# Optimization experiments

Measured on AMD Instinct MI355X. Metric: run time of the kernel, lower is better.

The kernel has to match this reference:

```python
import jax, jax.numpy as jnp
import numpy as np

T, B = 128, 64
EMB, HID, NTOK = 400, 1152, 33278
# layer dims: (in, out) per layer, matching AWD_LSTM construction
LAYER_DIMS = [(EMB, HID), (HID, HID), (HID, EMB)]


def _uniform(key, shape, bound):
    return jax.random.uniform(key, shape, jnp.float32, -bound, bound)


def setup_inputs() -> dict:
    key = jax.random.key(0)
    ks = jax.random.split(key, 32)
    inp = {
        "x": jax.random.normal(ks[0], (T, B, EMB), jnp.float32),
        "h0_0": jnp.zeros((B, HID), jnp.float32),
        "h0_1": jnp.zeros((B, HID), jnp.float32),
        "h0_2": jnp.zeros((B, EMB), jnp.float32),
        "c0_0": jnp.zeros((B, HID), jnp.float32),
        "c0_1": jnp.zeros((B, HID), jnp.float32),
        "c0_2": jnp.zeros((B, EMB), jnp.float32),
    }
    ki = 1
    for li, (din, dout) in enumerate(LAYER_DIMS):
        bound = 1.0 / np.sqrt(dout)
        inp[f"W_ih{li}"] = _uniform(ks[ki + 0], (4 * dout, din), bound)
        inp[f"W_hh{li}"] = _uniform(ks[ki + 1], (4 * dout, dout), bound)
        inp[f"b_ih{li}"] = _uniform(ks[ki + 2], (4 * dout,), bound)
        inp[f"b_hh{li}"] = _uniform(ks[ki + 3], (4 * dout,), bound)
        ki += 4
    bd = 1.0 / np.sqrt(EMB)
    inp["W_dec"] = _uniform(ks[ki], (NTOK, EMB), bd)
    inp["b_dec"] = _uniform(ks[ki + 1], (NTOK,), bd)
    return inp


def _lstm_cell(x, h, c, W_ih, W_hh, b_ih, b_hh):
    # PyTorch gate order: i, f, g, o
    gates = x @ W_ih.T + b_ih + h @ W_hh.T + b_hh
    i, f, g, o = jnp.split(gates, 4, axis=-1)
    c_new = jax.nn.sigmoid(f) * c + jax.nn.sigmoid(i) * jnp.tanh(g)
    h_new = jax.nn.sigmoid(o) * jnp.tanh(c_new)
    return h_new, c_new


def reference(x, h0_0, h0_1, h0_2, c0_0, c0_1, c0_2,
              W_ih0, W_hh0, b_ih0, b_hh0,
              W_ih1, W_hh1, b_ih1, b_hh1,
              W_ih2, W_hh2, b_ih2, b_hh2,
              W_dec, b_dec):
    params = [(W_ih0, W_hh0, b_ih0, b_hh0),
              (W_ih1, W_hh1, b_ih1, b_hh1),
              (W_ih2, W_hh2, b_ih2, b_hh2)]

    def step(carry, xt):
        hs, cs = carry
        inp = xt
        new_h, new_c = [], []
        for li in range(3):
            h, c = _lstm_cell(inp, hs[li], cs[li], *params[li])
            new_h.append(h)
            new_c.append(c)
            inp = h
        return (tuple(new_h), tuple(new_c)), new_h[-1]

    carry0 = ((h0_0, h0_1, h0_2), (c0_0, c0_1, c0_2))
    (hs, cs), out = jax.lax.scan(step, carry0, x)  # out: (T, B, EMB)
    decoded = out.reshape(T * B, EMB) @ W_dec.T + b_dec
    return decoded.reshape(T, B, NTOK)
```

## Files before the change

kernel.cpp:

```cpp
#include <hip/hip_runtime.h>
#include <math.h>

typedef unsigned short u16;
typedef __attribute__((ext_vector_type(8))) short short8;
typedef __attribute__((ext_vector_type(4))) float f32x4;
typedef __attribute__((ext_vector_type(2))) float f32x2;

__device__ __forceinline__ u16 f32_to_bf16(float x) {
    union { float f; unsigned int u; } v; v.f = x;
    unsigned int u = v.u;
    return (u16)((u + 0x7FFFu + ((u >> 16) & 1u)) >> 16);
}
__device__ __forceinline__ float bf16_to_f32(u16 h) {
    union { unsigned int u; float f; } v; v.u = ((unsigned int)h) << 16; return v.f;
}

__global__ void split_pad_kernel(const float* __restrict__ src,
                                 u16* __restrict__ hi, u16* __restrict__ lo,
                                 int N, int K, int Npad, int Kpad, int perm)
{
    int idx = blockIdx.x * 256 + threadIdx.x;
    if (idx >= Npad * Kpad) return;
    int n = idx / Kpad, k = idx - n * Kpad;
    float x = 0.f;
    if (n < N && k < K) {
        int srow = n;
        if (perm) { int dout = N >> 2; srow = (n & 3) * dout + (n >> 2); }
        x = src[(size_t)srow * K + k];
    }
    u16 h = f32_to_bf16(x);
    hi[idx] = h;
    lo[idx] = f32_to_bf16(x - bf16_to_f32(h));
}

__global__ void bias_perm_kernel(const float* __restrict__ bi,
                                 const float* __restrict__ bh,
                                 float* __restrict__ out, int N4)
{
    int c = blockIdx.x * 256 + threadIdx.x;
    if (c >= N4) return;
    int dout = N4 >> 2;
    int s = (c & 3) * dout + (c >> 2);
    out[c] = bi[s] + bh[s];
}

__global__ __launch_bounds__(256) void gemm3m(
    const float* __restrict__ Af32,
    const u16* __restrict__ Ahi, const u16* __restrict__ Alo,
    const u16* __restrict__ Whi, const u16* __restrict__ Wlo,
    const float* __restrict__ bias,
    float* __restrict__ C,
    int Nreal, int Kreal, int Kp, int lda, int ldc, int amode,
    int MT, int NSUB)
{
    extern __shared__ __align__(16) char smem[];
    u16 (*As)[128][32] = (u16 (*)[128][32])smem;
    u16 (*Ws)[128][32] = (u16 (*)[128][32])(smem + 16384);
    float (*Cs)[129]   = (float (*)[129])smem;

    const int tid  = threadIdx.x;
    const int lane = tid & 63, wave = tid >> 6;

    const int bid   = blockIdx.x;
    const int super = bid / (NSUB * MT);
    const int rem   = bid - super * (NSUB * MT);
    const int mtile = rem / NSUB;
    const int ntile = super * NSUB + (rem - mtile * NSUB);
    const int m0 = mtile * 128, n0 = ntile * 128;

    const int wm = (wave >> 1) * 64, wn = (wave & 1) * 64;

    f32x4 acc[4][4];
#pragma unroll
    for (int i = 0; i < 4; ++i)
#pragma unroll
        for (int j = 0; j < 4; ++j)
#pragma unroll
            for (int r = 0; r < 4; ++r) acc[i][j][r] = 0.f;

    const int srow = tid >> 2;
    const int sq   = tid & 3;
    const int dq   = (sq ^ ((srow >> 2) & 3)) * 8;
    const int fr   = lane & 15;
    const int fq   = lane >> 4;
    const int rcol = (fq ^ ((fr >> 2) & 3)) * 8;

    for (int k0 = 0; k0 < Kp; k0 += 32) {
#pragma unroll
        for (int half = 0; half < 2; ++half) {
            int row = half * 64 + srow;
            int kc  = k0 + sq * 8;
            if (amode == 0) {
                union { u16 s[8]; short8 v; } uh, ul;
                if (kc + 8 <= Kreal) {
                    const float* p = &Af32[(size_t)(m0 + row) * lda + kc];
#pragma unroll
                    for (int j = 0; j < 8; ++j) {
                        float xv = p[j];
                        u16 hh = f32_to_bf16(xv);
                        uh.s[j] = hh;
                        ul.s[j] = f32_to_bf16(xv - bf16_to_f32(hh));
                    }
                } else {
#pragma unroll
                    for (int j = 0; j < 8; ++j) { uh.s[j] = 0; ul.s[j] = 0; }
                }
                *(short8*)&As[0][row][dq] = uh.v;
                *(short8*)&As[1][row][dq] = ul.v;
            } else {
                size_t ao = (size_t)(m0 + row) * lda + kc;
                *(short8*)&As[0][row][dq] = *(const short8*)(Ahi + ao);
                *(short8*)&As[1][row][dq] = *(const short8*)(Alo + ao);
            }
            size_t wo = (size_t)(n0 + row) * Kp + kc;
            *(short8*)&Ws[0][row][dq] = *(const short8*)(Whi + wo);
            *(short8*)&Ws[1][row][dq] = *(const short8*)(Wlo + wo);
        }
        __syncthreads();

        short8 ah[4], al[4], wh[4], wl[4];
#pragma unroll
        for (int f = 0; f < 4; ++f) {
            int arow = wm + f * 16 + fr;
            ah[f] = *(const short8*)&As[0][arow][rcol];
            al[f] = *(const short8*)&As[1][arow][rcol];
            int wrow = wn + f * 16 + fr;
            wh[f] = *(const short8*)&Ws[0][wrow][rcol];
            wl[f] = *(const short8*)&Ws[1][wrow][rcol];
        }
#pragma unroll
        for (int i = 0; i < 4; ++i)
#pragma unroll
            for (int j = 0; j < 4; ++j) {
                acc[i][j] = __builtin_amdgcn_mfma_f32_16x16x32_bf16(ah[i], wh[j], acc[i][j], 0, 0, 0);
                acc[i][j] = __builtin_amdgcn_mfma_f32_16x16x32_bf16(ah[i], wl[j], acc[i][j], 0, 0, 0);
                acc[i][j] = __builtin_amdgcn_mfma_f32_16x16x32_bf16(al[i], wh[j], acc[i][j], 0, 0, 0);
            }
        __syncthreads();
    }

    const int erow = tid & 31;
    const int echk = tid >> 5;
    const int gm_base = m0 + ((erow >> 4) * 64) + (erow & 15);
    const int gn0 = n0 + echk * 16;
    const bool vec4ok = ((ldc & 3) == 0);

#pragma unroll
    for (int i = 0; i < 4; ++i) {
        __syncthreads();
#pragma unroll
        for (int j = 0; j < 4; ++j)
#pragma unroll
            for (int r = 0; r < 4; ++r)
                Cs[(wave >> 1) * 16 + fq * 4 + r][wn + j * 16 + fr] = acc[i][j][r];
        __syncthreads();

        const int gm = gm_base + i * 16;
        float* crow = C + (size_t)gm * ldc;
        if (gn0 + 16 <= Nreal) {
#pragma unroll
            for (int q = 0; q < 4; ++q) {
                f32x4 v = *(const f32x4*)&Cs[erow][echk * 16 + q * 4];
                if (bias) {
                    f32x4 bv = *(const f32x4*)&bias[gn0 + q * 4];
                    v += bv;
                }
                if (vec4ok) {
                    *(f32x4*)&crow[gn0 + q * 4] = v;
                } else {
                    f32x2 lo2 = {v[0], v[1]}, hi2 = {v[2], v[3]};
                    *(f32x2*)&crow[gn0 + q * 4]     = lo2;
                    *(f32x2*)&crow[gn0 + q * 4 + 2] = hi2;
                }
            }
        } else {
#pragma unroll
            for (int q = 0; q < 4; ++q)
#pragma unroll
                for (int p = 0; p < 4; ++p) {
                    int n = gn0 + q * 4 + p;
                    if (n < Nreal)
                        crow[n] = Cs[erow][echk * 16 + q * 4 + p] + (bias ? bias[n] : 0.f);
                }
        }
    }
}

#define PF(S, KT_) do {                                                        \
    int q_ = (((KT_) * 4 + fq) ^ sxor) * 8;                                    \
    a0h_##S = *(const short8*)&Wlds[rA * Kp + q_];                             \
    a0l_##S = *(const short8*)&Wlds[(32 + rA) * Kp + q_];                      \
    a1h_##S = *(const short8*)&Wlds[rB * Kp + q_];                             \
    a1l_##S = *(const short8*)&Wlds[(32 + rB) * Kp + q_];                      \
    hh_##S = *(const short8*)(hrow_hi + (KT_) * 32 + fq * 8);                  \
    hl_##S = *(const short8*)(hrow_lo + (KT_) * 32 + fq * 8);                  \
} while (0)

#define CM(S) do {                                                             \
    accA = __builtin_amdgcn_mfma_f32_16x16x32_bf16(a0h_##S, hh_##S, accA, 0, 0, 0); \
    accB = __builtin_amdgcn_mfma_f32_16x16x32_bf16(a1h_##S, hh_##S, accB, 0, 0, 0); \
    accA = __builtin_amdgcn_mfma_f32_16x16x32_bf16(a0h_##S, hl_##S, accA, 0, 0, 0); \
    accB = __builtin_amdgcn_mfma_f32_16x16x32_bf16(a1h_##S, hl_##S, accB, 0, 0, 0); \
    accA = __builtin_amdgcn_mfma_f32_16x16x32_bf16(a0l_##S, hh_##S, accA, 0, 0, 0); \
    accB = __builtin_amdgcn_mfma_f32_16x16x32_bf16(a1l_##S, hh_##S, accB, 0, 0, 0); \
} while (0)

__global__ __launch_bounds__(256, 1) void persistent_lstm(
    const u16* __restrict__ Whi, const u16* __restrict__ Wlo,
    const u16* __restrict__ h0hi, const u16* __restrict__ h0lo,
    u16* __restrict__ seqHi, u16* __restrict__ seqLo,
    const float* __restrict__ pre,
    const float* __restrict__ c_in, float* __restrict__ c_out,
    int* __restrict__ gcnt,
    int t0, int N4, int Kp, int dout, int G)
{
    extern __shared__ __align__(16) u16 Wlds[];
    const int tid  = threadIdx.x;
    const int lane = tid & 63, wave = tid >> 6;
    const int fr = lane & 15, fq = lane >> 4;
    const int c0blk = blockIdx.x * 32;
    const int CH = Kp >> 3;
    const int b = wave * 16 + fr;
    const int grp = blockIdx.x & 7;

    for (int idx = tid; idx < 64 * CH; idx += 256) {
        int buf = idx / (32 * CH);
        int rem = idx - buf * 32 * CH;
        int r = rem / CH, q = rem - r * CH;
        const u16* src = buf ? Wlo : Whi;
        short8 v = *(const short8*)(src + (size_t)(c0blk + r) * Kp + q * 8);
        *(short8*)&Wlds[(buf * 32 + r) * Kp + (q ^ (r & 7)) * 8] = v;
    }

    const int cA = c0blk + fq * 4;
    const int cB = cA + 16;
    const int jA = cA >> 2, jB = cB >> 2;
    float cregA = c_in[(size_t)b * dout + jA];
    float cregB = c_in[(size_t)b * dout + jB];

    const int rA = fr, rB = 16 + fr;
    const int sxor = fr & 7;
    const int KT = Kp >> 5;

    f32x4 preA = *(const f32x4*)(pre + (size_t)b * N4 + cA);
    f32x4 preB = *(const f32x4*)(pre + (size_t)b * N4 + cB);
    __syncthreads();

    for (int ts = 0; ts < 64; ++ts) {
        const int t = t0 + ts;
        const u16* hbase_hi = (t == 0) ? h0hi : seqHi + (size_t)(t - 1) * 64 * Kp;
        const u16* hbase_lo = (t == 0) ? h0lo : seqLo + (size_t)(t - 1) * 64 * Kp;
        const u16* hrow_hi = hbase_hi + (size_t)b * Kp;
        const u16* hrow_lo = hbase_lo + (size_t)b * Kp;

        f32x4 accA = {0.f, 0.f, 0.f, 0.f};
        f32x4 accB = {0.f, 0.f, 0.f, 0.f};
        short8 a0h_0, a0l_0, a1h_0, a1l_0, hh_0, hl_0;
        short8 a0h_1, a0l_1, a1h_1, a1l_1, hh_1, hl_1;
        short8 a0h_2, a0l_2, a1h_2, a1l_2, hh_2, hl_2;
        short8 a0h_3, a0l_3, a1h_3, a1l_3, hh_3, hl_3;
        short8 a0h_4, a0l_4, a1h_4, a1l_4, hh_4, hl_4;
        short8 a0h_5, a0l_5, a1h_5, a1l_5, hh_5, hl_5;

        PF(0, 0); PF(1, 1); PF(2, 2); PF(3, 3); PF(4, 4); PF(5, 5);
        for (int kt = 0; kt < KT - 6; kt += 6) {
            CM(0); PF(0, kt + 6);
            CM(1); PF(1, kt + 7);
            CM(2); PF(2, kt + 8);
            CM(3); PF(3, kt + 9);
            CM(4); PF(4, kt + 10);
            CM(5); PF(5, kt + 11);
        }
        CM(0); CM(1); CM(2); CM(3); CM(4); CM(5);

#pragma unroll
        for (int ct = 0; ct < 2; ++ct) {
            f32x4 a = ct ? accB : accA;
            f32x4 p = ct ? preB : preA;
            int j  = ct ? jB : jA;
            float gi = a[0] + p[0];
            float gf = a[1] + p[1];
            float gg = a[2] + p[2];
            float go_ = a[3] + p[3];
            float si = 1.f / (1.f + expf(-gi));
            float sf = 1.f / (1.f + expf(-gf));
            float so = 1.f / (1.f + expf(-go_));
            float tg = tanhf(gg);
            float cn = sf * (ct ? cregB : cregA) + si * tg;
            float hv = so * tanhf(cn);
            if (ct) cregB = cn; else cregA = cn;
            u16 hb = f32_to_bf16(hv);
            size_t so_ = (size_t)(t * 64 + b) * Kp + j;
            seqHi[so_] = hb;
            seqLo[so_] = f32_to_bf16(hv - bf16_to_f32(hb));
        }

        if (ts != 63) {
            __syncthreads();
            {
                const float* prow2 = pre + (size_t)((ts + 1) * 64 + b) * N4;
                preA = *(const f32x4*)(prow2 + cA);
                preB = *(const f32x4*)(prow2 + cB);
            }
            if (tid == 0) {
                __builtin_amdgcn_fence(__ATOMIC_RELEASE, "agent");
                __hip_atomic_fetch_add(&gcnt[(ts * 8 + grp) * 32], 1,
                                       __ATOMIC_RELAXED, __HIP_MEMORY_SCOPE_AGENT);
                int sum;
                do {
                    sum = 0;
#pragma unroll
                    for (int g = 0; g < 8; ++g)
                        sum += __hip_atomic_load(&gcnt[(ts * 8 + g) * 32],
                                                 __ATOMIC_RELAXED, __HIP_MEMORY_SCOPE_AGENT);
                    if (sum < G) __builtin_amdgcn_s_sleep(1);
                } while (sum < G);
            }
            __syncthreads();
            __builtin_amdgcn_sched_barrier(0);
        }
    }

    c_out[(size_t)b * dout + jA] = cregA;
    c_out[(size_t)b * dout + jB] = cregB;
}

extern "C" void kernel_launch(void* const* d_in, const int* in_sizes, int n_in,
                              void* d_out, int out_size, void* d_ws, size_t ws_size,
                              hipStream_t stream)
{
    const int T = 128, B = 64, EMB = 400, HID = 1152, NTOK = 33278;
    const int TB = T * B;

    const float* x     = (const float*)d_in[0];
    const float* h0[3] = {(const float*)d_in[1], (const float*)d_in[2], (const float*)d_in[3]};
    const float* c0[3] = {(const float*)d_in[4], (const float*)d_in[5], (const float*)d_in[6]};
    const float* W_ih[3] = {(const float*)d_in[7],  (const float*)d_in[11], (const float*)d_in[15]};
    const float* W_hh[3] = {(const float*)d_in[8],  (const float*)d_in[12], (const float*)d_in[16]};
    const float* b_ih[3] = {(const float*)d_in[9],  (const float*)d_in[13], (const float*)d_in[17]};
    const float* b_hh[3] = {(const float*)d_in[10], (const float*)d_in[14], (const float*)d_in[18]};
    const float* W_dec = (const float*)d_in[19];
    const float* b_dec = (const float*)d_in[20];

    const int din[3]    = {EMB, HID, HID};
    const int Kpre[3]   = {416, 1152, 1152};
    const int dh[3]     = {HID, HID, EMB};
    const int KpH[3]    = {1152, 1152, 576};
    const int N4[3]     = {4608, 4608, 1600};
    const int N4p128[3] = {4608, 4608, 1664};
    const int NSUBpre[3] = {6, 6, 13};
    const int Gp[3]     = {144, 144, 50};

    char* wsp = (char*)d_ws;
    size_t off = 0;
    auto alloc = [&](size_t bytes) -> char* {
        char* p = wsp + off; off = (off + bytes + 255) & ~(size_t)255; return p;
    };

    float* pre   = (float*)alloc((size_t)4096 * 4608 * 4);
    u16* seqHi   = (u16*)alloc((size_t)TB * 1152 * 2);
    u16* seqLo   = (u16*)alloc((size_t)TB * 1152 * 2);
    u16* WihHi   = (u16*)alloc((size_t)4608 * 1152 * 2);
    u16* WihLo   = (u16*)alloc((size_t)4608 * 1152 * 2);
    u16* WhhHi   = (u16*)alloc((size_t)4608 * 1152 * 2);
    u16* WhhLo   = (u16*)alloc((size_t)4608 * 1152 * 2);
    u16* h0Hi    = (u16*)alloc((size_t)B * 1152 * 2);
    u16* h0Lo    = (u16*)alloc((size_t)B * 1152 * 2);
    float* bsum  = (float*)alloc(4608 * 4);
    float* cstb  = (float*)alloc((size_t)B * HID * 4);
    const size_t gcntN = (size_t)6 * 64 * 8 * 32;
    int* gcnt = (int*)alloc(gcntN * 4);
    u16* WdecHi  = (u16*)pre;
    u16* WdecLo  = (u16*)pre + (size_t)33280 * 416;

    hipMemsetAsync(gcnt, 0, gcntN * 4, stream);
    hipFuncSetAttribute(reinterpret_cast<const void*>(persistent_lstm),
                        hipFuncAttributeMaxDynamicSharedMemorySize, 160 * 1024);
    hipFuncSetAttribute(reinterpret_cast<const void*>(gemm3m),
                        hipFuncAttributeMaxDynamicSharedMemorySize, 64 * 1024);

    auto run_split = [&](const float* src, u16* hi, u16* lo,
                         int N, int K, int Npad, int Kpad, int perm) {
        int total = Npad * Kpad;
        split_pad_kernel<<<(total + 255) / 256, 256, 0, stream>>>(
            src, hi, lo, N, K, Npad, Kpad, perm);
    };

    for (int l = 0; l < 3; ++l) {
        run_split(W_hh[l], WhhHi, WhhLo, N4[l], dh[l], N4[l], KpH[l], 1);
        run_split(h0[l], h0Hi, h0Lo, B, dh[l], B, KpH[l], 0);
        run_split(W_ih[l], WihHi, WihLo, N4[l], din[l], N4p128[l], Kpre[l], 1);
        bias_perm_kernel<<<(N4[l] + 255) / 256, 256, 0, stream>>>(
            b_ih[l], b_hh[l], bsum, N4[l]);

        const int ldaA = (l == 0) ? EMB : KpH[l - 1];
        const int NT = N4p128[l] / 128, MT = 32;
        const size_t ldsB = (size_t)128 * KpH[l];

        for (int halfT = 0; halfT < 2; ++halfT) {
            const int li = l * 2 + halfT;
            const float* Af32 = (l == 0) ? (x + (size_t)halfT * 4096 * EMB) : nullptr;
            const u16* Ah = (l == 0) ? nullptr : (seqHi + (size_t)halfT * 4096 * ldaA);
            const u16* Al = (l == 0) ? nullptr : (seqLo + (size_t)halfT * 4096 * ldaA);
            gemm3m<<<dim3(NT * MT), 256, 32768, stream>>>(
                Af32, Ah, Al, WihHi, WihLo, bsum, pre,
                N4[l], din[l], Kpre[l], ldaA, N4[l], (l == 0) ? 0 : 1,
                MT, NSUBpre[l]);

            const float* cin = (halfT == 0) ? c0[l] : cstb;
            persistent_lstm<<<dim3(Gp[l]), 256, ldsB, stream>>>(
                WhhHi, WhhLo, h0Hi, h0Lo, seqHi, seqLo, pre,
                cin, cstb,
                gcnt + (size_t)li * 64 * 8 * 32,
                halfT * 64, N4[l], KpH[l], dh[l], Gp[l]);
        }
    }

    run_split(W_dec, WdecHi, WdecLo, NTOK, EMB, 33280, 416, 0);
    gemm3m<<<dim3(260 * 64), 256, 32768, stream>>>(
        nullptr, seqHi, seqLo, WdecHi, WdecLo, b_dec, (float*)d_out,
        NTOK, EMB, 416, 576, NTOK, 1,
        64, 5);
}
```

Before: 6.536 ms.

## Use per-block flags, packed hi/lo hidden state, and LDS-direct loads in GEMM

Several changes land together. The LSTM grid barrier's grouped counters are replaced by one flag per block, each polled by its own thread. The hidden state is now stored as packed hi/lo u32 words written with atomic stores, so one load fetches both halves, and perm instructions split them apart. The GEMM's bf16 operand path now loads tiles directly into LDS through global_load_lds, one wave per buffer. The decoder GEMM's sub-tiling parameter also changes, and each step writes an extra sequence buffer, which adds memory traffic.

```diff
diff --git a/kernel.cpp b/kernel.cpp
--- a/kernel.cpp
+++ b/kernel.cpp
@@ -2,9 +2,11 @@
 #include <math.h>
 
 typedef unsigned short u16;
+typedef unsigned int u32;
 typedef __attribute__((ext_vector_type(8))) short short8;
 typedef __attribute__((ext_vector_type(4))) float f32x4;
 typedef __attribute__((ext_vector_type(2))) float f32x2;
+typedef __attribute__((ext_vector_type(4))) unsigned int u32x4;
 
 __device__ __forceinline__ u16 f32_to_bf16(float x) {
     union { float f; unsigned int u; } v; v.f = x;
@@ -13,6 +15,12 @@
 }
 __device__ __forceinline__ float bf16_to_f32(u16 h) {
     union { unsigned int u; float f; } v; v.u = ((unsigned int)h) << 16; return v.f;
+}
+
+__device__ __forceinline__ void gload16(const u16* g, u16* l) {
+    __builtin_amdgcn_global_load_lds(
+        (const __attribute__((address_space(1))) void*)g,
+        (__attribute__((address_space(3))) void*)l, 16, 0, 0);
 }
 
 __global__ void split_pad_kernel(const float* __restrict__ src,
@@ -33,6 +41,18 @@
     lo[idx] = f32_to_bf16(x - bf16_to_f32(h));
 }
 
+__global__ void pack_h0_kernel(const float* __restrict__ src, u32* __restrict__ dst,
+                               int Brows, int K, int Kpad)
+{
+    int idx = blockIdx.x * 256 + threadIdx.x;
+    if (idx >= Brows * Kpad) return;
+    int b = idx / Kpad, k = idx - b * Kpad;
+    float x = (k < K) ? src[(size_t)b * K + k] : 0.f;
+    u16 h = f32_to_bf16(x);
+    u16 l = f32_to_bf16(x - bf16_to_f32(h));
+    dst[idx] = (u32)h | ((u32)l << 16);
+}
+
 __global__ void bias_perm_kernel(const float* __restrict__ bi,
                                  const float* __restrict__ bh,
                                  float* __restrict__ out, int N4)
@@ -85,12 +105,23 @@
     const int fq   = lane >> 4;
     const int rcol = (fq ^ ((fr >> 2) & 3)) * 8;
 
+    const u16* gb = nullptr; u16* lb = nullptr; int gstr = 0;
+    if (amode != 0) {
+        u16* AsB = (u16*)smem;
+        u16* WsB = (u16*)(smem + 16384);
+        if (wave == 0)      { gb = Ahi + (size_t)m0 * lda; gstr = lda; lb = AsB; }
+        else if (wave == 1) { gb = Alo + (size_t)m0 * lda; gstr = lda; lb = AsB + 4096; }
+        else if (wave == 2) { gb = Whi + (size_t)n0 * Kp;  gstr = Kp;  lb = WsB; }
+        else                { gb = Wlo + (size_t)n0 * Kp;  gstr = Kp;  lb = WsB + 4096; }
+    }
+    const int lrow = lane >> 2, lq = lane & 3;
+
     for (int k0 = 0; k0 < Kp; k0 += 32) {
-#pragma unroll
-        for (int half = 0; half < 2; ++half) {
-            int row = half * 64 + srow;
-            int kc  = k0 + sq * 8;
-            if (amode == 0) {
+        if (amode == 0) {
+#pragma unroll
+            for (int half = 0; half < 2; ++half) {
+                int row = half * 64 + srow;
+                int kc  = k0 + sq * 8;
                 union { u16 s[8]; short8 v; } uh, ul;
                 if (kc + 8 <= Kreal) {
                     const float* p = &Af32[(size_t)(m0 + row) * lda + kc];
@@ -107,14 +138,17 @@
                 }
                 *(short8*)&As[0][row][dq] = uh.v;
                 *(short8*)&As[1][row][dq] = ul.v;
-            } else {
-                size_t ao = (size_t)(m0 + row) * lda + kc;
-                *(short8*)&As[0][row][dq] = *(const short8*)(Ahi + ao);
-                *(short8*)&As[1][row][dq] = *(const short8*)(Alo + ao);
-            }
-            size_t wo = (size_t)(n0 + row) * Kp + kc;
-            *(short8*)&Ws[0][row][dq] = *(const short8*)(Whi + wo);
-            *(short8*)&Ws[1][row][dq] = *(const short8*)(Wlo + wo);
+                size_t wo = (size_t)(n0 + row) * Kp + k0 + sq * 8;
+                *(short8*)&Ws[0][row][dq] = *(const short8*)(Whi + wo);
+                *(short8*)&Ws[1][row][dq] = *(const short8*)(Wlo + wo);
+            }
+        } else {
+#pragma unroll
+            for (int g = 0; g < 8; ++g) {
+                int row = g * 16 + lrow;
+                int srcq = lq ^ ((row >> 2) & 3);
+                gload16(gb + (size_t)row * gstr + k0 + srcq * 8, lb + g * 512);
+            }
         }
         __syncthreads();
 
@@ -192,8 +226,18 @@
     a0l_##S = *(const short8*)&Wlds[(32 + rA) * Kp + q_];                      \
     a1h_##S = *(const short8*)&Wlds[rB * Kp + q_];                             \
     a1l_##S = *(const short8*)&Wlds[(32 + rB) * Kp + q_];                      \
-    hh_##S = *(const short8*)(hrow_hi + (KT_) * 32 + fq * 8);                  \
-    hl_##S = *(const short8*)(hrow_lo + (KT_) * 32 + fq * 8);                  \
+    u32x4 u0_ = *(const u32x4*)(hrow + (KT_) * 32 + fq * 8);                   \
+    u32x4 u1_ = *(const u32x4*)(hrow + (KT_) * 32 + fq * 8 + 4);               \
+    union { short8 v; u32 d[4]; } H_, L_;                                      \
+    H_.d[0] = __builtin_amdgcn_perm(u0_[1], u0_[0], 0x05040100u);              \
+    L_.d[0] = __builtin_amdgcn_perm(u0_[1], u0_[0], 0x07060302u);              \
+    H_.d[1] = __builtin_amdgcn_perm(u0_[3], u0_[2], 0x05040100u);              \
+    L_.d[1] = __builtin_amdgcn_perm(u0_[3], u0_[2], 0x07060302u);              \
+    H_.d[2] = __builtin_amdgcn_perm(u1_[1], u1_[0], 0x05040100u);              \
+    L_.d[2] = __builtin_amdgcn_perm(u1_[1], u1_[0], 0x07060302u);              \
+    H_.d[3] = __builtin_amdgcn_perm(u1_[3], u1_[2], 0x05040100u);              \
+    L_.d[3] = __builtin_amdgcn_perm(u1_[3], u1_[2], 0x07060302u);              \
+    hh_##S = H_.v; hl_##S = L_.v;                                              \
 } while (0)
 
 #define CM(S) do {                                                             \
@@ -207,11 +251,12 @@
 
 __global__ __launch_bounds__(256, 1) void persistent_lstm(
     const u16* __restrict__ Whi, const u16* __restrict__ Wlo,
-    const u16* __restrict__ h0hi, const u16* __restrict__ h0lo,
+    const u32* __restrict__ h0HL,
+    u32* __restrict__ seqHL,
     u16* __restrict__ seqHi, u16* __restrict__ seqLo,
     const float* __restrict__ pre,
     const float* __restrict__ c_in, float* __restrict__ c_out,
-    int* __restrict__ gcnt,
+    int* __restrict__ flags,
     int t0, int N4, int Kp, int dout, int G)
 {
     extern __shared__ __align__(16) u16 Wlds[];
@@ -221,7 +266,6 @@
     const int c0blk = blockIdx.x * 32;
     const int CH = Kp >> 3;
     const int b = wave * 16 + fr;
-    const int grp = blockIdx.x & 7;
 
     for (int idx = tid; idx < 64 * CH; idx += 256) {
         int buf = idx / (32 * CH);
@@ -248,10 +292,8 @@
 
     for (int ts = 0; ts < 64; ++ts) {
         const int t = t0 + ts;
-        const u16* hbase_hi = (t == 0) ? h0hi : seqHi + (size_t)(t - 1) * 64 * Kp;
-        const u16* hbase_lo = (t == 0) ? h0lo : seqLo + (size_t)(t - 1) * 64 * Kp;
-        const u16* hrow_hi = hbase_hi + (size_t)b * Kp;
-        const u16* hrow_lo = hbase_lo + (size_t)b * Kp;
+        const u32* hbase = (t == 0) ? h0HL : seqHL + (size_t)(t - 1) * 64 * Kp;
+        const u32* hrow = hbase + (size_t)b * Kp;
 
         f32x4 accA = {0.f, 0.f, 0.f, 0.f};
         f32x4 accB = {0.f, 0.f, 0.f, 0.f};
@@ -290,9 +332,13 @@
             float hv = so * tanhf(cn);
             if (ct) cregB = cn; else cregA = cn;
             u16 hb = f32_to_bf16(hv);
+            u16 lb = f32_to_bf16(hv - bf16_to_f32(hb));
+            __hip_atomic_store(&seqHL[(size_t)(t * 64 + b) * Kp + j],
+                               (u32)hb | ((u32)lb << 16),
+                               __ATOMIC_RELAXED, __HIP_MEMORY_SCOPE_AGENT);
             size_t so_ = (size_t)(t * 64 + b) * Kp + j;
             seqHi[so_] = hb;
-            seqLo[so_] = f32_to_bf16(hv - bf16_to_f32(hb));
+            seqLo[so_] = lb;
         }
 
         if (ts != 63) {
@@ -302,19 +348,13 @@
                 preA = *(const f32x4*)(prow2 + cA);
                 preB = *(const f32x4*)(prow2 + cB);
             }
-            if (tid == 0) {
-                __builtin_amdgcn_fence(__ATOMIC_RELEASE, "agent");
-                __hip_atomic_fetch_add(&gcnt[(ts * 8 + grp) * 32], 1,
-                                       __ATOMIC_RELAXED, __HIP_MEMORY_SCOPE_AGENT);
-                int sum;
-                do {
-                    sum = 0;
-#pragma unroll
-                    for (int g = 0; g < 8; ++g)
-                        sum += __hip_atomic_load(&gcnt[(ts * 8 + g) * 32],
-                                                 __ATOMIC_RELAXED, __HIP_MEMORY_SCOPE_AGENT);
-                    if (sum < G) __builtin_amdgcn_s_sleep(1);
-                } while (sum < G);
+            if (tid == 0)
+                __hip_atomic_store(&flags[blockIdx.x], ts + 1,
+                                   __ATOMIC_RELAXED, __HIP_MEMORY_SCOPE_AGENT);
+            if (tid < G) {
+                while (__hip_atomic_load(&flags[tid], __ATOMIC_RELAXED,
+                                         __HIP_MEMORY_SCOPE_AGENT) < ts + 1)
+                    __builtin_amdgcn_s_sleep(1);
             }
             __syncthreads();
             __builtin_amdgcn_sched_barrier(0);
@@ -360,20 +400,19 @@
     float* pre   = (float*)alloc((size_t)4096 * 4608 * 4);
     u16* seqHi   = (u16*)alloc((size_t)TB * 1152 * 2);
     u16* seqLo   = (u16*)alloc((size_t)TB * 1152 * 2);
+    u32* seqHL   = (u32*)alloc((size_t)TB * 1152 * 4);
     u16* WihHi   = (u16*)alloc((size_t)4608 * 1152 * 2);
     u16* WihLo   = (u16*)alloc((size_t)4608 * 1152 * 2);
     u16* WhhHi   = (u16*)alloc((size_t)4608 * 1152 * 2);
     u16* WhhLo   = (u16*)alloc((size_t)4608 * 1152 * 2);
-    u16* h0Hi    = (u16*)alloc((size_t)B * 1152 * 2);
-    u16* h0Lo    = (u16*)alloc((size_t)B * 1152 * 2);
+    u32* h0HL    = (u32*)alloc((size_t)B * 1152 * 4);
     float* bsum  = (float*)alloc(4608 * 4);
     float* cstb  = (float*)alloc((size_t)B * HID * 4);
-    const size_t gcntN = (size_t)6 * 64 * 8 * 32;
-    int* gcnt = (int*)alloc(gcntN * 4);
+    int* flags   = (int*)alloc(6 * 256 * 4);
     u16* WdecHi  = (u16*)pre;
     u16* WdecLo  = (u16*)pre + (size_t)33280 * 416;
 
-    hipMemsetAsync(gcnt, 0, gcntN * 4, stream);
+    hipMemsetAsync(flags, 0, 6 * 256 * 4, stream);
     hipFuncSetAttribute(reinterpret_cast<const void*>(persistent_lstm),
                         hipFuncAttributeMaxDynamicSharedMemorySize, 160 * 1024);
     hipFuncSetAttribute(reinterpret_cast<const void*>(gemm3m),
@@ -388,7 +427,8 @@
 
     for (int l = 0; l < 3; ++l) {
         run_split(W_hh[l], WhhHi, WhhLo, N4[l], dh[l], N4[l], KpH[l], 1);
-        run_split(h0[l], h0Hi, h0Lo, B, dh[l], B, KpH[l], 0);
+        pack_h0_kernel<<<(B * KpH[l] + 255) / 256, 256, 0, stream>>>(
+            h0[l], h0HL, B, dh[l], KpH[l]);
         run_split(W_ih[l], WihHi, WihLo, N4[l], din[l], N4p128[l], Kpre[l], 1);
         bias_perm_kernel<<<(N4[l] + 255) / 256, 256, 0, stream>>>(
             b_ih[l], b_hh[l], bsum, N4[l]);
@@ -409,9 +449,8 @@
 
             const float* cin = (halfT == 0) ? c0[l] : cstb;
             persistent_lstm<<<dim3(Gp[l]), 256, ldsB, stream>>>(
-                WhhHi, WhhLo, h0Hi, h0Lo, seqHi, seqLo, pre,
-                cin, cstb,
-                gcnt + (size_t)li * 64 * 8 * 32,
+                WhhHi, WhhLo, h0HL, seqHL, seqHi, seqLo, pre,
+                cin, cstb, flags + li * 256,
                 halfT * 64, N4[l], KpH[l], dh[l], Gp[l]);
         }
     }
@@ -420,5 +459,5 @@
     gemm3m<<<dim3(260 * 64), 256, 32768, stream>>>(
         nullptr, seqHi, seqLo, WdecHi, WdecLo, b_dec, (float*)d_out,
         NTOK, EMB, 416, 576, NTOK, 1,
-        64, 5);
-}
+        64, 13);
+}
```

Result: slower. 6.998 ms (+7.1%).
